# Kernel optimization log

Hardware: AMD Instinct MI355X
Metric: run time of the kernel (lower is better)

Reference implementation:

```python
import jax, jax.numpy as jnp
import numpy as np


def setup_inputs() -> dict:
    key = jax.random.key(0)
    k_user, k_music, k_label, k_mem, k_w = jax.random.split(key, 5)
    B, H, N = 65536, 1024, 256  # batch, hidden (=2*hidden_size), memory slots
    user = jax.random.normal(k_user, (B, H), dtype=jnp.float32)
    music = jax.random.normal(k_music, (B, H), dtype=jnp.float32)
    memory = jax.random.normal(k_mem, (N, H), dtype=jnp.float32) * (1.0 / np.sqrt(H).astype(np.float32))
    W_out = jax.random.normal(k_w, (H, 2), dtype=jnp.float32) * (1.0 / np.sqrt(H).astype(np.float32))
    b_out = jnp.zeros((2,), dtype=jnp.float32)
    label = jax.random.randint(k_label, (B,), 0, 2, dtype=jnp.int64 if jax.config.jax_enable_x64 else jnp.int32)
    return {"user": user, "music": music, "memory": memory, "W_out": W_out, "b_out": b_out, "label": label}


def reference(user, music, memory, W_out, b_out, label):
    # s = user * music  (elementwise interaction)  [B, H]
    s = user * music
    # classification head: Linear(hidden, 2)
    out_result = s @ W_out + b_out  # [B, 2]
    # memory read: softmax(s @ memory^T) @ memory
    attn = jax.nn.softmax(s @ memory.T, axis=1)  # [B, N]
    rel = attn @ memory  # [B, H]
    # translational score: ||user + rel - music||_2 per row
    diff = user + rel - music
    score = jnp.sqrt(jnp.sum(diff * diff, axis=1))  # [B]
    mask = (2 * label - 1).astype(score.dtype)  # {-1, +1}
    loss = jnp.mean(mask * score)
    return loss, out_result
```

## Files before the change

### kernel.cpp

```cpp
#include <hip/hip_runtime.h>
#include <hip/hip_bf16.h>

typedef float ff4 __attribute__((ext_vector_type(4)));
typedef short s8v __attribute__((ext_vector_type(8)));
typedef unsigned int u4v __attribute__((ext_vector_type(4)));
typedef unsigned int u2v __attribute__((ext_vector_type(2)));

#define Hd 1024
#define Nn 256
#define KC 32
#define NCHUNK 32
#define RB 32
#define SSTR 40

__device__ __forceinline__ unsigned bf16r(float f) {
    unsigned u = __builtin_bit_cast(unsigned, f);
    return (u + 0x7FFFu + ((u >> 16) & 1u)) >> 16;
}

__device__ __forceinline__ unsigned cvtpk(float lo, float hi) {
    unsigned r;
    asm("v_cvt_pk_bf16_f32 %0, %1, %2" : "=v"(r) : "v"(lo), "v"(hi));
    return r;
}

__device__ __forceinline__ void glds16(void* lds, const void* g) {
    __builtin_amdgcn_global_load_lds(
        (const __attribute__((address_space(1))) unsigned int*)g,
        (__attribute__((address_space(3))) unsigned int*)lds, 16, 0, 0);
}

__global__ void conv_mem_kernel(const float* __restrict__ mem, unsigned short* __restrict__ memB) {
    int g = blockIdx.x * 256 + threadIdx.x;
    int b = g & 3;
    int r = (g >> 2) & 255;
    int c = g >> 10;
    const float* src = mem + (size_t)r * Hd + c * KC + b * 8;
    ff4 a0 = *(const ff4*)src;
    ff4 a1 = *(const ff4*)(src + 4);
    u4v v;
    v[0] = bf16r(a0[0]) | (bf16r(a0[1]) << 16);
    v[1] = bf16r(a0[2]) | (bf16r(a0[3]) << 16);
    v[2] = bf16r(a1[0]) | (bf16r(a1[1]) << 16);
    v[3] = bf16r(a1[2]) | (bf16r(a1[3]) << 16);
    size_t dst = (size_t)c * 16384 + (size_t)r * 64 + (size_t)((b ^ ((r >> 1) & 3)) * 16);
    *(u4v*)((char*)memB + dst) = v;
}

__global__ void conv_w_kernel(const float* __restrict__ Wout, unsigned short* __restrict__ Wbf) {
    int t = threadIdx.x;
    int c = t >> 7;
    int h0 = (t & 127) * 8;
    u4v v;
#pragma unroll
    for (int j = 0; j < 4; ++j) {
        unsigned lo = bf16r(Wout[(h0 + 2 * j) * 2 + c]);
        unsigned hi = bf16r(Wout[(h0 + 2 * j + 1) * 2 + c]);
        v[j] = lo | (hi << 16);
    }
    *(u4v*)(Wbf + (size_t)c * Hd + h0) = v;
}

__global__ __launch_bounds__(256) void gram_kernel(const float* __restrict__ mem,
                                                   unsigned short* __restrict__ Gbf) {
    __shared__ float LA[32][132];
    __shared__ float LB[32][132];
    const int t = threadIdx.x;
    const int bi = blockIdx.x >> 3, bj = blockIdx.x & 7;
    const int j = t & 31, i0 = t >> 5;
    float acc0 = 0.f, acc1 = 0.f, acc2 = 0.f, acc3 = 0.f;
    for (int kc = 0; kc < Hd; kc += 128) {
        __syncthreads();
#pragma unroll
        for (int q = 0; q < 4; ++q) {
            int c = t + q * 256;
            int r = c >> 5, fc = (c & 31) << 2;
            *(ff4*)&LA[r][fc] = *(const ff4*)(mem + (size_t)(bi * 32 + r) * Hd + kc + fc);
            *(ff4*)&LB[r][fc] = *(const ff4*)(mem + (size_t)(bj * 32 + r) * Hd + kc + fc);
        }
        __syncthreads();
#pragma unroll 4
        for (int kk = 0; kk < 128; kk += 4) {
            ff4 b = *(const ff4*)&LB[j][kk];
            ff4 a0 = *(const ff4*)&LA[i0][kk];
            ff4 a1 = *(const ff4*)&LA[i0 + 8][kk];
            ff4 a2 = *(const ff4*)&LA[i0 + 16][kk];
            ff4 a3 = *(const ff4*)&LA[i0 + 24][kk];
            acc0 += a0[0]*b[0] + a0[1]*b[1] + a0[2]*b[2] + a0[3]*b[3];
            acc1 += a1[0]*b[0] + a1[1]*b[1] + a1[2]*b[2] + a1[3]*b[3];
            acc2 += a2[0]*b[0] + a2[1]*b[1] + a2[2]*b[2] + a2[3]*b[3];
            acc3 += a3[0]*b[0] + a3[1]*b[1] + a3[2]*b[2] + a3[3]*b[3];
        }
    }
    const int gj = bj * 32 + j;
    Gbf[(size_t)(bi * 32 + i0 +  0) * Nn + gj] = (unsigned short)bf16r(acc0);
    Gbf[(size_t)(bi * 32 + i0 +  8) * Nn + gj] = (unsigned short)bf16r(acc1);
    Gbf[(size_t)(bi * 32 + i0 + 16) * Nn + gj] = (unsigned short)bf16r(acc2);
    Gbf[(size_t)(bi * 32 + i0 + 24) * Nn + gj] = (unsigned short)bf16r(acc3);
}

__global__ __launch_bounds__(256, 4) void fused_kernel(
    const float* __restrict__ user, const float* __restrict__ music,
    const float* __restrict__ bout, const int* __restrict__ label,
    const unsigned short* __restrict__ memB,
    const unsigned short* __restrict__ Wbf,
    const unsigned short* __restrict__ Gbf,
    float* __restrict__ out, float* __restrict__ partials)
{
    __shared__ __align__(16) unsigned char smem[39168];
    unsigned short* sS = (unsigned short*)(smem + 32768);
    unsigned short* sD = (unsigned short*)(smem + 35328);
    float* fMax   = (float*)(smem + 37888);
    float* fSum   = fMax + 64;
    float* fCross = fMax + 128;
    float* fQuad  = fMax + 192;
    float* fAux   = fMax + 256;
    unsigned short* sAttn = (unsigned short*)smem;

    const int t = threadIdx.x;
    const int w = t >> 6;
    const int l = t & 63;
    const int la = l & 15, lb = l >> 4;
    const int g = w >> 1;
    const int h = w & 1;
    const int row0 = blockIdx.x * RB;

    const int sr = t >> 3, kp = t & 7;
    const float* uR = user  + (size_t)(row0 + sr) * Hd + kp * 4;
    const float* mR = music + (size_t)(row0 + sr) * Hd + kp * 4;
    const char* gsrcW = (const char*)memB + w * 4096 + l * 16;
    const unsigned short* wrowB = Wbf + (size_t)(la < 2 ? la : 1) * Hd + lb * 8;

    const int arow = (g * 16 + la) * SSTR + lb * 8;
    const int moff = h * 8192 + la * 64 + ((lb ^ ((la >> 1) & 3)) << 4);

    ff4 accL[8], accD[8];
#pragma unroll
    for (int i = 0; i < 8; ++i) { accL[i] = (ff4)0.0f; accD[i] = (ff4)0.0f; }
    ff4 accH = (ff4)0.0f;
    float sd2 = 0.f;

#pragma unroll
    for (int i = 0; i < 4; ++i)
        glds16(smem + w * 4096 + i * 1024, gsrcW + i * 1024);
    {
        ff4 uv = *(const ff4*)(uR);
        ff4 mv = *(const ff4*)(mR);
        float d0 = uv[0]-mv[0], d1 = uv[1]-mv[1], d2 = uv[2]-mv[2], d3 = uv[3]-mv[3];
        sd2 = fmaf(d0,d0,sd2); sd2 = fmaf(d1,d1,sd2); sd2 = fmaf(d2,d2,sd2); sd2 = fmaf(d3,d3,sd2);
        u2v vs, vd;
        vs[0] = cvtpk(uv[0]*mv[0], uv[1]*mv[1]); vs[1] = cvtpk(uv[2]*mv[2], uv[3]*mv[3]);
        vd[0] = cvtpk(d0, d1);                   vd[1] = cvtpk(d2, d3);
        *(u2v*)(sS + sr * SSTR + kp * 4) = vs;
        *(u2v*)(sD + sr * SSTR + kp * 4) = vd;
    }
    __syncthreads();

    for (int c = 0; c < NCHUNK; ++c) {
        const int p = c & 1;
        s8v fs = *(const s8v*)(sS + arow);
        s8v fd = *(const s8v*)(sD + arow);
        s8v bW = *(const s8v*)(wrowB + c * KC);
        ff4 nuv, nmv;
        if (c + 1 < NCHUNK) {
#pragma unroll
            for (int i = 0; i < 4; ++i)
                glds16(smem + (p ^ 1) * 16384 + w * 4096 + i * 1024,
                       gsrcW + (size_t)(c + 1) * 16384 + i * 1024);
            nuv = *(const ff4*)(uR + (c + 1) * KC);
            nmv = *(const ff4*)(mR + (c + 1) * KC);
        }
        __syncthreads();
        {
            const unsigned char* mbase = smem + p * 16384;
#pragma unroll
            for (int nt = 0; nt < 8; ++nt) {
                s8v bM = *(const s8v*)(mbase + nt * 1024 + moff);
                accL[nt] = __builtin_amdgcn_mfma_f32_16x16x32_bf16(fs, bM, accL[nt], 0, 0, 0);
                accD[nt] = __builtin_amdgcn_mfma_f32_16x16x32_bf16(fd, bM, accD[nt], 0, 0, 0);
            }
            accH = __builtin_amdgcn_mfma_f32_16x16x32_bf16(fs, bW, accH, 0, 0, 0);
        }
        if (c + 1 < NCHUNK) {
            float d0 = nuv[0]-nmv[0], d1 = nuv[1]-nmv[1], d2 = nuv[2]-nmv[2], d3 = nuv[3]-nmv[3];
            sd2 = fmaf(d0,d0,sd2); sd2 = fmaf(d1,d1,sd2); sd2 = fmaf(d2,d2,sd2); sd2 = fmaf(d3,d3,sd2);
            u2v vs, vd;
            vs[0] = cvtpk(nuv[0]*nmv[0], nuv[1]*nmv[1]); vs[1] = cvtpk(nuv[2]*nmv[2], nuv[3]*nmv[3]);
            vd[0] = cvtpk(d0, d1);                       vd[1] = cvtpk(d2, d3);
            *(u2v*)(sS + sr * SSTR + kp * 4) = vs;
            *(u2v*)(sD + sr * SSTR + kp * 4) = vd;
        }
        __syncthreads();
    }

    if (h == 0 && la < 2) {
#pragma unroll
        for (int j = 0; j < 4; ++j) {
            int gr = row0 + g * 16 + lb * 4 + j;
            out[1 + gr * 2 + la] = accH[j] + bout[la];
        }
    }
    sd2 += __shfl_xor(sd2, 1);
    sd2 += __shfl_xor(sd2, 2);
    sd2 += __shfl_xor(sd2, 4);
    if (kp == 0) fAux[sr] = sd2;

    ff4 mx = accL[0];
#pragma unroll
    for (int nt = 1; nt < 8; ++nt) {
        mx[0] = fmaxf(mx[0], accL[nt][0]); mx[1] = fmaxf(mx[1], accL[nt][1]);
        mx[2] = fmaxf(mx[2], accL[nt][2]); mx[3] = fmaxf(mx[3], accL[nt][3]);
    }
#pragma unroll
    for (int s = 1; s < 16; s <<= 1) {
        mx[0] = fmaxf(mx[0], __shfl_xor(mx[0], s));
        mx[1] = fmaxf(mx[1], __shfl_xor(mx[1], s));
        mx[2] = fmaxf(mx[2], __shfl_xor(mx[2], s));
        mx[3] = fmaxf(mx[3], __shfl_xor(mx[3], s));
    }
    ff4 sm = (ff4)0.0f;
#pragma unroll
    for (int nt = 0; nt < 8; ++nt) {
        sm[0] += __expf(accL[nt][0] - mx[0]); sm[1] += __expf(accL[nt][1] - mx[1]);
        sm[2] += __expf(accL[nt][2] - mx[2]); sm[3] += __expf(accL[nt][3] - mx[3]);
    }
#pragma unroll
    for (int s = 1; s < 16; s <<= 1) {
        sm[0] += __shfl_xor(sm[0], s); sm[1] += __shfl_xor(sm[1], s);
        sm[2] += __shfl_xor(sm[2], s); sm[3] += __shfl_xor(sm[3], s);
    }
    if (la < 4) {
        const int grow = g * 16 + lb * 4 + la;
        float mv = (la == 0) ? mx[0] : (la == 1) ? mx[1] : (la == 2) ? mx[2] : mx[3];
        float sv = (la == 0) ? sm[0] : (la == 1) ? sm[1] : (la == 2) ? sm[2] : sm[3];
        fMax[h * 32 + grow] = mv;
        fSum[h * 32 + grow] = sv;
    }
    __syncthreads();

    ff4 Mr, Dinv;
#pragma unroll
    for (int j = 0; j < 4; ++j) {
        const int grow = g * 16 + lb * 4 + j;
        float m0 = fMax[grow], m1 = fMax[32 + grow];
        float M = fmaxf(m0, m1);
        float den = fSum[grow] * __expf(m0 - M) + fSum[32 + grow] * __expf(m1 - M);
        Mr[j] = M; Dinv[j] = 1.0f / den;
    }
    ff4 cross = (ff4)0.0f;
#pragma unroll
    for (int nt = 0; nt < 8; ++nt) {
        accL[nt][0] = __expf(accL[nt][0] - Mr[0]) * Dinv[0];
        accL[nt][1] = __expf(accL[nt][1] - Mr[1]) * Dinv[1];
        accL[nt][2] = __expf(accL[nt][2] - Mr[2]) * Dinv[2];
        accL[nt][3] = __expf(accL[nt][3] - Mr[3]) * Dinv[3];
        cross[0] = fmaf(accL[nt][0], accD[nt][0], cross[0]);
        cross[1] = fmaf(accL[nt][1], accD[nt][1], cross[1]);
        cross[2] = fmaf(accL[nt][2], accD[nt][2], cross[2]);
        cross[3] = fmaf(accL[nt][3], accD[nt][3], cross[3]);
    }
#pragma unroll
    for (int s = 1; s < 16; s <<= 1) {
        cross[0] += __shfl_xor(cross[0], s); cross[1] += __shfl_xor(cross[1], s);
        cross[2] += __shfl_xor(cross[2], s); cross[3] += __shfl_xor(cross[3], s);
    }
    if (la < 4) {
        const int grow = g * 16 + lb * 4 + la;
        float cv = (la == 0) ? cross[0] : (la == 1) ? cross[1] : (la == 2) ? cross[2] : cross[3];
        fCross[h * 32 + grow] = cv;
    }
    {
        const int rb = lb << 2;
#pragma unroll
        for (int nt = 0; nt < 8; ++nt) {
            const int cc = h * 128 + nt * 16 + la;
            sAttn[(g * 16 + rb + 0) * 264 + cc] = (unsigned short)bf16r(accL[nt][0]);
            sAttn[(g * 16 + rb + 1) * 264 + cc] = (unsigned short)bf16r(accL[nt][1]);
            sAttn[(g * 16 + rb + 2) * 264 + cc] = (unsigned short)bf16r(accL[nt][2]);
            sAttn[(g * 16 + rb + 3) * 264 + cc] = (unsigned short)bf16r(accL[nt][3]);
        }
    }
    __syncthreads();

    ff4 accG[8];
#pragma unroll
    for (int i = 0; i < 8; ++i) accG[i] = (ff4)0.0f;
#pragma unroll
    for (int ks = 0; ks < 8; ++ks) {
        s8v aA = *(const s8v*)(sAttn + (g * 16 + la) * 264 + ks * 32 + lb * 8);
#pragma unroll
        for (int nt = 0; nt < 8; ++nt) {
            s8v bG = *(const s8v*)(Gbf + (size_t)(h * 128 + nt * 16 + la) * Nn + ks * 32 + lb * 8);
            accG[nt] = __builtin_amdgcn_mfma_f32_16x16x32_bf16(aA, bG, accG[nt], 0, 0, 0);
        }
    }
    ff4 quad = (ff4)0.0f;
#pragma unroll
    for (int nt = 0; nt < 8; ++nt) {
        quad[0] = fmaf(accL[nt][0], accG[nt][0], quad[0]);
        quad[1] = fmaf(accL[nt][1], accG[nt][1], quad[1]);
        quad[2] = fmaf(accL[nt][2], accG[nt][2], quad[2]);
        quad[3] = fmaf(accL[nt][3], accG[nt][3], quad[3]);
    }
#pragma unroll
    for (int s = 1; s < 16; s <<= 1) {
        quad[0] += __shfl_xor(quad[0], s); quad[1] += __shfl_xor(quad[1], s);
        quad[2] += __shfl_xor(quad[2], s); quad[3] += __shfl_xor(quad[3], s);
    }
    if (la < 4) {
        const int grow = g * 16 + lb * 4 + la;
        float qv = (la == 0) ? quad[0] : (la == 1) ? quad[1] : (la == 2) ? quad[2] : quad[3];
        fQuad[h * 32 + grow] = qv;
    }
    __syncthreads();

    float val = 0.f;
    if (h == 0 && la < 4) {
        const int grow = g * 16 + lb * 4 + la;
        float s2 = fAux[grow] + 2.0f * (fCross[grow] + fCross[32 + grow])
                 + (fQuad[grow] + fQuad[32 + grow]);
        float sc = sqrtf(fmaxf(s2, 0.0f));
        const int gr = row0 + grow;
        val = (float)(2 * label[gr] - 1) * sc;
    }
#pragma unroll
    for (int s = 1; s < 64; s <<= 1) val += __shfl_xor(val, s);
    if (l == 0) partials[blockIdx.x * 4 + w] = val;
}

__global__ void finalize_kernel(const float* __restrict__ partials, float* __restrict__ out,
                                int np, float invB) {
    const int t = threadIdx.x;
    float v = 0.f;
    for (int i = t; i < np; i += 256) v += partials[i];
#pragma unroll
    for (int s = 1; s < 64; s <<= 1) v += __shfl_xor(v, s);
    __shared__ float ws4[4];
    if ((t & 63) == 0) ws4[t >> 6] = v;
    __syncthreads();
    if (t == 0) out[0] = (ws4[0] + ws4[1] + ws4[2] + ws4[3]) * invB;
}

extern "C" void kernel_launch(void* const* d_in, const int* in_sizes, int n_in,
                              void* d_out, int out_size, void* d_ws, size_t ws_size,
                              hipStream_t stream) {
    const float* user  = (const float*)d_in[0];
    const float* music = (const float*)d_in[1];
    const float* mem   = (const float*)d_in[2];
    const float* Wout  = (const float*)d_in[3];
    const float* bout  = (const float*)d_in[4];
    const int*   label = (const int*)d_in[5];
    const int Bn   = in_sizes[0] / Hd;
    const int nblk = Bn / RB;

    unsigned short* memB = (unsigned short*)d_ws;
    unsigned short* Wbf  = (unsigned short*)((char*)d_ws + 524288);
    unsigned short* Gbf  = (unsigned short*)((char*)d_ws + 524288 + 4096);
    float* partials      = (float*)((char*)d_ws + 524288 + 4096 + 131072);

    conv_mem_kernel<<<128, 256, 0, stream>>>(mem, memB);
    conv_w_kernel<<<1, 256, 0, stream>>>(Wout, Wbf);
    gram_kernel<<<64, 256, 0, stream>>>(mem, Gbf);
    fused_kernel<<<nblk, 256, 0, stream>>>(user, music, bout, label, memB, Wbf, Gbf,
                                           (float*)d_out, partials);
    finalize_kernel<<<1, 256, 0, stream>>>(partials, (float*)d_out, nblk * 4, 1.0f / (float)Bn);
}
```

Before: 221.8 us.

## Load MFMA fragments directly from global, drop LDS staging and block barriers

The main loop no longer stages memory tiles and the s/d fragments in LDS behind two barriers per chunk. Each lane loads its user/music slice and its memory B-fragments straight from global or L2, using a new chunk-major memory and Gram layout so the per-lane fragment loads are contiguous. User/music loads are software-prefetched two chunks deep, and the head MFMA runs only on the h==0 waves. The cost is redundant global/L2 traffic, since two waves now load the same user/music rows and every wave loads memory fragments on its own. Register pressure also rises, and launch bounds drop from 4 to 3 blocks per SIMD.

```diff
diff --git a/kernel.cpp b/kernel.cpp
--- a/kernel.cpp
+++ b/kernel.cpp
@@ -4,14 +4,12 @@
 typedef float ff4 __attribute__((ext_vector_type(4)));
 typedef short s8v __attribute__((ext_vector_type(8)));
 typedef unsigned int u4v __attribute__((ext_vector_type(4)));
-typedef unsigned int u2v __attribute__((ext_vector_type(2)));
 
 #define Hd 1024
 #define Nn 256
 #define KC 32
 #define NCHUNK 32
 #define RB 32
-#define SSTR 40
 
 __device__ __forceinline__ unsigned bf16r(float f) {
     unsigned u = __builtin_bit_cast(unsigned, f);
@@ -22,12 +20,6 @@
     unsigned r;
     asm("v_cvt_pk_bf16_f32 %0, %1, %2" : "=v"(r) : "v"(lo), "v"(hi));
     return r;
-}
-
-__device__ __forceinline__ void glds16(void* lds, const void* g) {
-    __builtin_amdgcn_global_load_lds(
-        (const __attribute__((address_space(1))) unsigned int*)g,
-        (__attribute__((address_space(3))) unsigned int*)lds, 16, 0, 0);
 }
 
 __global__ void conv_mem_kernel(const float* __restrict__ mem, unsigned short* __restrict__ memB) {
@@ -43,8 +35,7 @@
     v[1] = bf16r(a0[2]) | (bf16r(a0[3]) << 16);
     v[2] = bf16r(a1[0]) | (bf16r(a1[1]) << 16);
     v[3] = bf16r(a1[2]) | (bf16r(a1[3]) << 16);
-    size_t dst = (size_t)c * 16384 + (size_t)r * 64 + (size_t)((b ^ ((r >> 1) & 3)) * 16);
-    *(u4v*)((char*)memB + dst) = v;
+    *(u4v*)(memB + (size_t)c * 8192 + (size_t)r * 32 + b * 8) = v;
 }
 
 __global__ void conv_w_kernel(const float* __restrict__ Wout, unsigned short* __restrict__ Wbf) {
@@ -62,7 +53,7 @@
 }
 
 __global__ __launch_bounds__(256) void gram_kernel(const float* __restrict__ mem,
-                                                   unsigned short* __restrict__ Gbf) {
+                                                   unsigned short* __restrict__ Gcm) {
     __shared__ float LA[32][132];
     __shared__ float LB[32][132];
     const int t = threadIdx.x;
@@ -92,30 +83,23 @@
             acc3 += a3[0]*b[0] + a3[1]*b[1] + a3[2]*b[2] + a3[3]*b[3];
         }
     }
-    const int gj = bj * 32 + j;
-    Gbf[(size_t)(bi * 32 + i0 +  0) * Nn + gj] = (unsigned short)bf16r(acc0);
-    Gbf[(size_t)(bi * 32 + i0 +  8) * Nn + gj] = (unsigned short)bf16r(acc1);
-    Gbf[(size_t)(bi * 32 + i0 + 16) * Nn + gj] = (unsigned short)bf16r(acc2);
-    Gbf[(size_t)(bi * 32 + i0 + 24) * Nn + gj] = (unsigned short)bf16r(acc3);
-}
-
-__global__ __launch_bounds__(256, 4) void fused_kernel(
+    const size_t base = (size_t)bj * 8192 + (size_t)j;
+    Gcm[base + (size_t)(bi * 32 + i0 +  0) * 32] = (unsigned short)bf16r(acc0);
+    Gcm[base + (size_t)(bi * 32 + i0 +  8) * 32] = (unsigned short)bf16r(acc1);
+    Gcm[base + (size_t)(bi * 32 + i0 + 16) * 32] = (unsigned short)bf16r(acc2);
+    Gcm[base + (size_t)(bi * 32 + i0 + 24) * 32] = (unsigned short)bf16r(acc3);
+}
+
+__global__ __launch_bounds__(256, 3) void fused_kernel(
     const float* __restrict__ user, const float* __restrict__ music,
     const float* __restrict__ bout, const int* __restrict__ label,
     const unsigned short* __restrict__ memB,
     const unsigned short* __restrict__ Wbf,
-    const unsigned short* __restrict__ Gbf,
+    const unsigned short* __restrict__ Gcm,
     float* __restrict__ out, float* __restrict__ partials)
 {
-    __shared__ __align__(16) unsigned char smem[39168];
-    unsigned short* sS = (unsigned short*)(smem + 32768);
-    unsigned short* sD = (unsigned short*)(smem + 35328);
-    float* fMax   = (float*)(smem + 37888);
-    float* fSum   = fMax + 64;
-    float* fCross = fMax + 128;
-    float* fQuad  = fMax + 192;
-    float* fAux   = fMax + 256;
-    unsigned short* sAttn = (unsigned short*)smem;
+    __shared__ __align__(16) unsigned short sAttn[32 * 264];
+    __shared__ float fMax[64], fSum[64], fCross[64], fQuad[64], fAux[32];
 
     const int t = threadIdx.x;
     const int w = t >> 6;
@@ -124,15 +108,13 @@
     const int g = w >> 1;
     const int h = w & 1;
     const int row0 = blockIdx.x * RB;
-
-    const int sr = t >> 3, kp = t & 7;
-    const float* uR = user  + (size_t)(row0 + sr) * Hd + kp * 4;
-    const float* mR = music + (size_t)(row0 + sr) * Hd + kp * 4;
-    const char* gsrcW = (const char*)memB + w * 4096 + l * 16;
+    const int myrow = row0 + g * 16 + la;
+
+    const float* uR = user  + (size_t)myrow * Hd + lb * 8;
+    const float* mR = music + (size_t)myrow * Hd + lb * 8;
+    const unsigned short* fbase = memB + h * 4096 + la * 32 + lb * 8;
     const unsigned short* wrowB = Wbf + (size_t)(la < 2 ? la : 1) * Hd + lb * 8;
-
-    const int arow = (g * 16 + la) * SSTR + lb * 8;
-    const int moff = h * 8192 + la * 64 + ((lb ^ ((la >> 1) & 3)) << 4);
+    const unsigned short* gbase = Gcm + h * 4096 + la * 32 + lb * 8;
 
     ff4 accL[8], accD[8];
 #pragma unroll
@@ -140,58 +122,53 @@
     ff4 accH = (ff4)0.0f;
     float sd2 = 0.f;
 
-#pragma unroll
-    for (int i = 0; i < 4; ++i)
-        glds16(smem + w * 4096 + i * 1024, gsrcW + i * 1024);
-    {
-        ff4 uv = *(const ff4*)(uR);
-        ff4 mv = *(const ff4*)(mR);
-        float d0 = uv[0]-mv[0], d1 = uv[1]-mv[1], d2 = uv[2]-mv[2], d3 = uv[3]-mv[3];
-        sd2 = fmaf(d0,d0,sd2); sd2 = fmaf(d1,d1,sd2); sd2 = fmaf(d2,d2,sd2); sd2 = fmaf(d3,d3,sd2);
-        u2v vs, vd;
-        vs[0] = cvtpk(uv[0]*mv[0], uv[1]*mv[1]); vs[1] = cvtpk(uv[2]*mv[2], uv[3]*mv[3]);
-        vd[0] = cvtpk(d0, d1);                   vd[1] = cvtpk(d2, d3);
-        *(u2v*)(sS + sr * SSTR + kp * 4) = vs;
-        *(u2v*)(sD + sr * SSTR + kp * 4) = vd;
-    }
-    __syncthreads();
-
-    for (int c = 0; c < NCHUNK; ++c) {
-        const int p = c & 1;
-        s8v fs = *(const s8v*)(sS + arow);
-        s8v fd = *(const s8v*)(sD + arow);
-        s8v bW = *(const s8v*)(wrowB + c * KC);
-        ff4 nuv, nmv;
-        if (c + 1 < NCHUNK) {
-#pragma unroll
-            for (int i = 0; i < 4; ++i)
-                glds16(smem + (p ^ 1) * 16384 + w * 4096 + i * 1024,
-                       gsrcW + (size_t)(c + 1) * 16384 + i * 1024);
-            nuv = *(const ff4*)(uR + (c + 1) * KC);
-            nmv = *(const ff4*)(mR + (c + 1) * KC);
-        }
-        __syncthreads();
-        {
-            const unsigned char* mbase = smem + p * 16384;
-#pragma unroll
-            for (int nt = 0; nt < 8; ++nt) {
-                s8v bM = *(const s8v*)(mbase + nt * 1024 + moff);
-                accL[nt] = __builtin_amdgcn_mfma_f32_16x16x32_bf16(fs, bM, accL[nt], 0, 0, 0);
-                accD[nt] = __builtin_amdgcn_mfma_f32_16x16x32_bf16(fd, bM, accD[nt], 0, 0, 0);
-            }
-            accH = __builtin_amdgcn_mfma_f32_16x16x32_bf16(fs, bW, accH, 0, 0, 0);
-        }
-        if (c + 1 < NCHUNK) {
-            float d0 = nuv[0]-nmv[0], d1 = nuv[1]-nmv[1], d2 = nuv[2]-nmv[2], d3 = nuv[3]-nmv[3];
-            sd2 = fmaf(d0,d0,sd2); sd2 = fmaf(d1,d1,sd2); sd2 = fmaf(d2,d2,sd2); sd2 = fmaf(d3,d3,sd2);
-            u2v vs, vd;
-            vs[0] = cvtpk(nuv[0]*nmv[0], nuv[1]*nmv[1]); vs[1] = cvtpk(nuv[2]*nmv[2], nuv[3]*nmv[3]);
-            vd[0] = cvtpk(d0, d1);                       vd[1] = cvtpk(d2, d3);
-            *(u2v*)(sS + sr * SSTR + kp * 4) = vs;
-            *(u2v*)(sD + sr * SSTR + kp * 4) = vd;
-        }
-        __syncthreads();
-    }
+#define STEP(K, UA, UB, MA, MB)                                                 \
+    {                                                                           \
+        float s0 = UA[0]*MA[0], s1 = UA[1]*MA[1], s2 = UA[2]*MA[2], s3 = UA[3]*MA[3]; \
+        float s4 = UB[0]*MB[0], s5 = UB[1]*MB[1], s6 = UB[2]*MB[2], s7 = UB[3]*MB[3]; \
+        float d0 = UA[0]-MA[0], d1 = UA[1]-MA[1], d2 = UA[2]-MA[2], d3 = UA[3]-MA[3]; \
+        float d4 = UB[0]-MB[0], d5 = UB[1]-MB[1], d6 = UB[2]-MB[2], d7 = UB[3]-MB[3]; \
+        sd2 = fmaf(d0,d0,sd2); sd2 = fmaf(d1,d1,sd2); sd2 = fmaf(d2,d2,sd2); sd2 = fmaf(d3,d3,sd2); \
+        sd2 = fmaf(d4,d4,sd2); sd2 = fmaf(d5,d5,sd2); sd2 = fmaf(d6,d6,sd2); sd2 = fmaf(d7,d7,sd2); \
+        u4v ps, pd;                                                             \
+        ps[0] = cvtpk(s0,s1); ps[1] = cvtpk(s2,s3); ps[2] = cvtpk(s4,s5); ps[3] = cvtpk(s6,s7); \
+        pd[0] = cvtpk(d0,d1); pd[1] = cvtpk(d2,d3); pd[2] = cvtpk(d4,d5); pd[3] = cvtpk(d6,d7); \
+        s8v fs = __builtin_bit_cast(s8v, ps);                                   \
+        s8v fd = __builtin_bit_cast(s8v, pd);                                   \
+        const unsigned short* fp = fbase + (size_t)(K) * 8192;                  \
+        s8v bM[8];                                                              \
+        _Pragma("unroll")                                                       \
+        for (int nt = 0; nt < 8; ++nt) bM[nt] = *(const s8v*)(fp + nt * 512);   \
+        _Pragma("unroll")                                                       \
+        for (int nt = 0; nt < 8; ++nt) {                                        \
+            accL[nt] = __builtin_amdgcn_mfma_f32_16x16x32_bf16(fs, bM[nt], accL[nt], 0, 0, 0); \
+            accD[nt] = __builtin_amdgcn_mfma_f32_16x16x32_bf16(fd, bM[nt], accD[nt], 0, 0, 0); \
+        }                                                                       \
+        if (h == 0) {                                                           \
+            s8v bW = *(const s8v*)(wrowB + (K) * KC);                           \
+            accH = __builtin_amdgcn_mfma_f32_16x16x32_bf16(fs, bW, accH, 0, 0, 0); \
+        }                                                                       \
+    }
+
+    ff4 ua0 = *(const ff4*)(uR);
+    ff4 ub0 = *(const ff4*)(uR + 4);
+    ff4 ma0 = *(const ff4*)(mR);
+    ff4 mb0 = *(const ff4*)(mR + 4);
+    for (int k = 0; k < NCHUNK; k += 2) {
+        ff4 ua1 = *(const ff4*)(uR + (k + 1) * KC);
+        ff4 ub1 = *(const ff4*)(uR + (k + 1) * KC + 4);
+        ff4 ma1 = *(const ff4*)(mR + (k + 1) * KC);
+        ff4 mb1 = *(const ff4*)(mR + (k + 1) * KC + 4);
+        STEP(k, ua0, ub0, ma0, mb0)
+        if (k + 2 < NCHUNK) {
+            ua0 = *(const ff4*)(uR + (k + 2) * KC);
+            ub0 = *(const ff4*)(uR + (k + 2) * KC + 4);
+            ma0 = *(const ff4*)(mR + (k + 2) * KC);
+            mb0 = *(const ff4*)(mR + (k + 2) * KC + 4);
+        }
+        STEP(k + 1, ua1, ub1, ma1, mb1)
+    }
+#undef STEP
 
     if (h == 0 && la < 2) {
 #pragma unroll
@@ -200,10 +177,9 @@
             out[1 + gr * 2 + la] = accH[j] + bout[la];
         }
     }
-    sd2 += __shfl_xor(sd2, 1);
-    sd2 += __shfl_xor(sd2, 2);
-    sd2 += __shfl_xor(sd2, 4);
-    if (kp == 0) fAux[sr] = sd2;
+    sd2 += __shfl_xor(sd2, 16);
+    sd2 += __shfl_xor(sd2, 32);
+    if (h == 0 && lb == 0) fAux[g * 16 + la] = sd2;
 
     ff4 mx = accL[0];
 #pragma unroll
@@ -288,9 +264,10 @@
 #pragma unroll
     for (int ks = 0; ks < 8; ++ks) {
         s8v aA = *(const s8v*)(sAttn + (g * 16 + la) * 264 + ks * 32 + lb * 8);
+        const unsigned short* gp = gbase + (size_t)ks * 8192;
 #pragma unroll
         for (int nt = 0; nt < 8; ++nt) {
-            s8v bG = *(const s8v*)(Gbf + (size_t)(h * 128 + nt * 16 + la) * Nn + ks * 32 + lb * 8);
+            s8v bG = *(const s8v*)(gp + nt * 512);
             accG[nt] = __builtin_amdgcn_mfma_f32_16x16x32_bf16(aA, bG, accG[nt], 0, 0, 0);
         }
     }
@@ -355,13 +332,13 @@
 
     unsigned short* memB = (unsigned short*)d_ws;
     unsigned short* Wbf  = (unsigned short*)((char*)d_ws + 524288);
-    unsigned short* Gbf  = (unsigned short*)((char*)d_ws + 524288 + 4096);
+    unsigned short* Gcm  = (unsigned short*)((char*)d_ws + 524288 + 4096);
     float* partials      = (float*)((char*)d_ws + 524288 + 4096 + 131072);
 
     conv_mem_kernel<<<128, 256, 0, stream>>>(mem, memB);
     conv_w_kernel<<<1, 256, 0, stream>>>(Wout, Wbf);
-    gram_kernel<<<64, 256, 0, stream>>>(mem, Gbf);
-    fused_kernel<<<nblk, 256, 0, stream>>>(user, music, bout, label, memB, Wbf, Gbf,
+    gram_kernel<<<64, 256, 0, stream>>>(mem, Gcm);
+    fused_kernel<<<nblk, 256, 0, stream>>>(user, music, bout, label, memB, Wbf, Gcm,
                                            (float*)d_out, partials);
     finalize_kernel<<<1, 256, 0, stream>>>(partials, (float*)d_out, nblk * 4, 1.0f / (float)Bn);
 }
```

Result: slower. 378.0 us (+70.4%).
